# Kernel tuning notes

Hardware: AMD Instinct MI355X
Metric: run time of the kernel (lower is better)

Reference implementation:

```python
import jax, jax.numpy as jnp
import numpy as np

B, L, DIM, HEADS = 2, 2048, 1536, 12
HD = DIM // HEADS  # 128
C = HD // 2        # 64 rotary pairs
EPS = 1e-6


def setup_inputs() -> dict:
    key = jax.random.key(0)
    ks = jax.random.split(key, 8)
    x = jax.random.normal(ks[0], (B, L, DIM), jnp.float32)
    # ragged grids: sample0 fills L, sample1 has 2*24*32 = 1536 valid tokens
    grid_sizes = jnp.array([[2, 32, 32], [2, 24, 32]], dtype=jnp.int32)
    seq_lens = jnp.array([2048, 1536], dtype=jnp.int32)
    # rope freqs table [1024, C] (cos/sin of pos * inv_freq)
    pos = jnp.arange(1024, dtype=jnp.float32)[:, None]
    inv = 1.0 / (10000.0 ** (jnp.arange(C, dtype=jnp.float32) / C))
    ang = pos * inv
    freqs_cos, freqs_sin = jnp.cos(ang), jnp.sin(ang)
    init = lambda k: jax.random.normal(k, (DIM, DIM), jnp.float32) / np.sqrt(DIM)
    return dict(
        x=x, seq_lens=seq_lens, grid_sizes=grid_sizes,
        freqs_cos=freqs_cos, freqs_sin=freqs_sin,
        Wq=init(ks[1]), bq=jnp.zeros((DIM,), jnp.float32),
        Wk=init(ks[2]), bk=jnp.zeros((DIM,), jnp.float32),
        Wv=init(ks[3]), bv=jnp.zeros((DIM,), jnp.float32),
        Wo=init(ks[4]), bo=jnp.zeros((DIM,), jnp.float32),
        gq=jnp.ones((DIM,), jnp.float32), gk=jnp.ones((DIM,), jnp.float32),
    )


def _rope_one(xb, grid, cos, sin):
    # xb: [L, n, d]; grid: (f, h, w); cos/sin: [1024, C]
    f, h, w = grid[0], grid[1], grid[2]
    c = cos.shape[1]
    c2 = c // 3
    c1 = c - 2 * c2  # freqs split [c1, c2, c2] over axes (f, h, w)
    p = jnp.arange(xb.shape[0])
    hw = h * w
    valid = p < f * hw
    fi = jnp.where(valid, p // hw, 0)
    hi = jnp.where(valid, (p // w) % h, 0)
    wi = jnp.where(valid, p % w, 0)
    cos_p = jnp.concatenate([cos[fi, :c1], cos[hi, c1:c1 + c2], cos[wi, c1 + c2:]], axis=-1)
    sin_p = jnp.concatenate([sin[fi, :c1], sin[hi, c1:c1 + c2], sin[wi, c1 + c2:]], axis=-1)
    # positions beyond seq_len pass through unrotated (identity rotation)
    cos_p = jnp.where(valid[:, None], cos_p, 1.0)[:, None, :]  # [L,1,C]
    sin_p = jnp.where(valid[:, None], sin_p, 0.0)[:, None, :]
    xr, xi = xb[..., 0::2], xb[..., 1::2]
    out_r = xr * cos_p - xi * sin_p
    out_i = xr * sin_p + xi * cos_p
    return jnp.stack([out_r, out_i], axis=-1).reshape(xb.shape)


_rope_apply = jax.vmap(_rope_one, in_axes=(0, 0, None, None))


def _rms(t, g):
    t32 = t.astype(jnp.float32)
    return (t32 * jax.lax.rsqrt(jnp.mean(t32 * t32, axis=-1, keepdims=True) + EPS) * g).astype(t.dtype)


def reference(x, seq_lens, grid_sizes, freqs_cos, freqs_sin,
              Wq, bq, Wk, bk, Wv, bv, Wo, bo, gq, gk):
    b, s = x.shape[:2]
    n, d = HEADS, HD
    q = _rms(x @ Wq + bq, gq).reshape(b, s, n, d)
    k = _rms(x @ Wk + bk, gk).reshape(b, s, n, d)
    v = (x @ Wv + bv).reshape(b, s, n, d)
    q = _rope_apply(q, grid_sizes, freqs_cos, freqs_sin)
    k = _rope_apply(k, grid_sizes, freqs_cos, freqs_sin)
    scale = 1.0 / np.sqrt(d).astype(np.float32)
    scores = jnp.einsum('bqnd,bknd->bnqk', q, k) * scale
    kmask = jnp.arange(s)[None, :] < seq_lens[:, None]  # [b, s] key validity
    scores = jnp.where(kmask[:, None, None, :], scores, jnp.float32(-1e9))
    attn = jax.nn.softmax(scores, axis=-1)
    out = jnp.einsum('bnqk,bknd->bqnd', attn, v).reshape(b, s, n * d)
    return out @ Wo + bo
```

## Files before the change

### kernel.cpp

```cpp
#include <hip/hip_runtime.h>
#include <hip/hip_bf16.h>

#define DIM   1536
#define HEADS 12
#define HD    128
#define LSEQ  2048
#define NB    2
#define NTOK  (NB*LSEQ)

using f32x4 = __attribute__((ext_vector_type(4))) float;
using s16x8 = __attribute__((ext_vector_type(8))) short;
using u16x4 = __attribute__((ext_vector_type(4))) unsigned short;

__device__ __forceinline__ unsigned short f2bf(float f) {
  unsigned int u = __builtin_bit_cast(unsigned int, f);
  u += 0x7fffu + ((u >> 16) & 1u);
  return (unsigned short)(u >> 16);
}
__device__ __forceinline__ float bf2f(unsigned short u) {
  return __builtin_bit_cast(float, (unsigned int)u << 16);
}
__device__ __forceinline__ void gload_lds16(const void* g, void* l) {
  __builtin_amdgcn_global_load_lds(
      (__attribute__((address_space(1))) void*)const_cast<void*>(g),
      (__attribute__((address_space(3))) void*)l,
      16, 0, 0);
}

__global__ __launch_bounds__(256) void cvt_x(const float* __restrict__ x,
                                             unsigned short* __restrict__ xb, int n) {
  int i = (blockIdx.x * 256 + threadIdx.x) * 4;
  int stride = gridDim.x * 256 * 4;
  for (; i < n; i += stride) {
    f32x4 v = *(const f32x4*)(x + i);
    u16x4 o;
    o[0] = f2bf(v[0]); o[1] = f2bf(v[1]); o[2] = f2bf(v[2]); o[3] = f2bf(v[3]);
    *(u16x4*)(xb + i) = o;
  }
}

__global__ __launch_bounds__(256) void wtrans(const float* W0, const float* W1,
                                              const float* W2, const float* W3,
                                              unsigned short* __restrict__ Wt) {
  const float* W = blockIdx.z == 0 ? W0 : blockIdx.z == 1 ? W1 : blockIdx.z == 2 ? W2 : W3;
  unsigned short* out = Wt + (size_t)blockIdx.z * DIM * DIM;
  const int n0 = blockIdx.x * 64, k0 = blockIdx.y * 64;
  __shared__ unsigned short t[64][68];
  const int tid = threadIdx.x;
#pragma unroll
  for (int i = 0; i < 16; i++) {
    int idx = tid + i * 256;
    int r = idx >> 6, c = idx & 63;
    t[r][c] = f2bf(W[(size_t)(k0 + r) * DIM + n0 + c]);
  }
  __syncthreads();
#pragma unroll
  for (int i = 0; i < 16; i++) {
    int idx = tid + i * 256;
    int r = idx >> 6, c = idx & 63;
    out[(size_t)(n0 + r) * DIM + k0 + c] = t[c][r];
  }
}

__global__ __launch_bounds__(256) void gemm_bt(
    const unsigned short* __restrict__ A, const unsigned short* __restrict__ Bt,
    void* __restrict__ Cv,
    const float* __restrict__ b0, const float* __restrict__ b1, const float* __restrict__ b2,
    int M, int N, int K, int biasMode, int outBf16) {
  __shared__ __align__(16) unsigned short As[128 * 64];
  __shared__ __align__(16) unsigned short Bs[128 * 64];
  const int tid = threadIdx.x;
  const int lane = tid & 63, w = tid >> 6;
  const int wr = w >> 1, wc = w & 1;
  const int l15 = lane & 15, g4 = lane >> 4;
  const int nwg = gridDim.x * gridDim.y;
  const int bidf = blockIdx.y * gridDim.x + blockIdx.x;
  const int cpx = nwg >> 3;
  const int sw = (bidf & 7) * cpx + (bidf >> 3);
  const int m0 = (sw / gridDim.x) * 128, n0 = (sw % gridDim.x) * 128;

  f32x4 acc[4][4];
#pragma unroll
  for (int i = 0; i < 4; i++)
#pragma unroll
    for (int j = 0; j < 4; j++) acc[i][j] = (f32x4){0.f, 0.f, 0.f, 0.f};

  for (int kt = 0; kt < K; kt += 64) {
    __syncthreads();
#pragma unroll
    for (int i = 0; i < 4; i++) {
      int c = tid + i * 256;
      int row = c >> 3, g = c & 7;
      int gs = g ^ (row & 7);
      gload_lds16(A + (size_t)(m0 + row) * K + kt + gs * 8, As + c * 8);
    }
#pragma unroll
    for (int i = 0; i < 4; i++) {
      int c = tid + i * 256;
      int row = c >> 3, g = c & 7;
      int gs = g ^ (row & 7);
      gload_lds16(Bt + (size_t)(n0 + row) * K + kt + gs * 8, Bs + c * 8);
    }
    __syncthreads();
#pragma unroll
    for (int kk = 0; kk < 2; kk++) {
      s16x8 af[4], bfr[4];
#pragma unroll
      for (int m = 0; m < 4; m++) {
        int row = wr * 64 + m * 16 + l15;
        int off = row * 128 + ((kk * 64 + g4 * 16) ^ ((row & 7) << 4));
        af[m] = *(const s16x8*)((const char*)As + off);
      }
#pragma unroll
      for (int n = 0; n < 4; n++) {
        int row = wc * 64 + n * 16 + l15;
        int off = row * 128 + ((kk * 64 + g4 * 16) ^ ((row & 7) << 4));
        bfr[n] = *(const s16x8*)((const char*)Bs + off);
      }
#pragma unroll
      for (int m = 0; m < 4; m++)
#pragma unroll
        for (int n = 0; n < 4; n++)
          acc[m][n] = __builtin_amdgcn_mfma_f32_16x16x32_bf16(af[m], bfr[n], acc[m][n], 0, 0, 0);
    }
  }
#pragma unroll
  for (int m = 0; m < 4; m++)
#pragma unroll
    for (int n = 0; n < 4; n++)
#pragma unroll
      for (int r = 0; r < 4; r++) {
        int grow = m0 + wr * 64 + m * 16 + g4 * 4 + r;
        int gcol = n0 + wc * 64 + n * 16 + l15;
        float bias = (biasMode == 1)
                         ? b0[gcol]
                         : (gcol < 1536 ? b0[gcol]
                                        : (gcol < 3072 ? b1[gcol - 1536] : b2[gcol - 3072]));
        float val = acc[m][n][r] + bias;
        if (outBf16) ((unsigned short*)Cv)[(size_t)grow * N + gcol] = f2bf(val);
        else         ((float*)Cv)[(size_t)grow * N + gcol] = val;
      }
}

__global__ __launch_bounds__(256) void rmsrope(
    const unsigned short* __restrict__ qkvb,
    const float* __restrict__ gq, const float* __restrict__ gk,
    const int* __restrict__ grid_sizes,
    const float* __restrict__ fcos, const float* __restrict__ fsin,
    unsigned short* __restrict__ qb, unsigned short* __restrict__ kb) {
  const int t = blockIdx.x;
  const int b = t >> 11, l = t & 2047;
  const int tid = threadIdx.x;
  __shared__ float qrow[1536], krow[1536];
  __shared__ float red[8];
  const unsigned short* rq = qkvb + (size_t)t * 4608;
  const unsigned short* rk = rq + 1536;
  float sq = 0.f, sk = 0.f;
  if (tid < 192) {
    s16x8 vq = *(const s16x8*)(rq + tid * 8);
    s16x8 vk = *(const s16x8*)(rk + tid * 8);
#pragma unroll
    for (int j = 0; j < 8; j++) {
      float a = bf2f((unsigned short)vq[j]); qrow[tid * 8 + j] = a; sq += a * a;
      float c = bf2f((unsigned short)vk[j]); krow[tid * 8 + j] = c; sk += c * c;
    }
  }
  for (int o = 32; o; o >>= 1) { sq += __shfl_down(sq, o); sk += __shfl_down(sk, o); }
  if ((tid & 63) == 0) { red[tid >> 6] = sq; red[4 + (tid >> 6)] = sk; }
  __syncthreads();
  const float rsq = rsqrtf((red[0] + red[1] + red[2] + red[3]) * (1.f / 1536.f) + 1e-6f);
  const float rsk = rsqrtf((red[4] + red[5] + red[6] + red[7]) * (1.f / 1536.f) + 1e-6f);
  const float QS = 0.08838834764831845f;
  const int fg = grid_sizes[b * 3 + 0], hg = grid_sizes[b * 3 + 1], wg = grid_sizes[b * 3 + 2];
  const int hw = hg * wg;
  const bool valid = l < fg * hw;
  const int fi = valid ? l / hw : 0;
  const int hi = valid ? (l / wg) % hg : 0;
  const int wi = valid ? l % wg : 0;
  const size_t obase = (((size_t)b * HEADS) * LSEQ + l) * HD;
  for (int i = tid; i < HEADS * 64; i += 256) {
    int hd = i >> 6, j = i & 63;
    float c, s;
    if (valid) {
      int idx = j < 22 ? fi : (j < 43 ? hi : wi);
      c = fcos[idx * 64 + j]; s = fsin[idx * 64 + j];
    } else { c = 1.f; s = 0.f; }
    int col = hd * 128 + 2 * j;
    size_t o = obase + (size_t)hd * LSEQ * HD + 2 * j;
    float xr = qrow[col] * rsq * gq[col];
    float xi = qrow[col + 1] * rsq * gq[col + 1];
    float q0 = (xr * c - xi * s) * QS, q1 = (xr * s + xi * c) * QS;
    *(unsigned int*)(qb + o) = (unsigned int)f2bf(q0) | ((unsigned int)f2bf(q1) << 16);
    xr = krow[col] * rsk * gk[col];
    xi = krow[col + 1] * rsk * gk[col + 1];
    *(unsigned int*)(kb + o) =
        (unsigned int)f2bf(xr * c - xi * s) | ((unsigned int)f2bf(xr * s + xi * c) << 16);
  }
}

__global__ __launch_bounds__(256) void vtrans(const unsigned short* __restrict__ qkvb,
                                              unsigned short* __restrict__ vt) {
  const int lt = blockIdx.x, h = blockIdx.y, b = blockIdx.z;
  const int l0 = lt * 64;
  __shared__ unsigned short tile[64][130];
  const int tid = threadIdx.x;
#pragma unroll
  for (int i = 0; i < 4; i++) {
    int idx = tid + i * 256;
    int tk = idx >> 4, dc = (idx & 15) * 8;
    s16x8 v = *(const s16x8*)(qkvb + (size_t)(b * 2048 + l0 + tk) * 4608 + 3072 + h * 128 + dc);
#pragma unroll
    for (int j = 0; j < 8; j++) tile[tk][dc + j] = (unsigned short)v[j];
  }
  __syncthreads();
  const size_t ob = (((size_t)b * HEADS + h) * HD) * LSEQ + l0;
#pragma unroll
  for (int i = 0; i < 4; i++) {
    int idx = tid + i * 256;
    int d = idx >> 3, ck = (idx & 7) * 8;
    s16x8 o;
#pragma unroll
    for (int j = 0; j < 8; j++) o[j] = (short)tile[ck + j][d];
    *(s16x8*)(vt + ob + (size_t)d * LSEQ + ck) = o;
  }
}

__global__ __launch_bounds__(256) void flash(
    const unsigned short* __restrict__ qb, const unsigned short* __restrict__ kb,
    const unsigned short* __restrict__ vt, const int* __restrict__ seq_lens,
    unsigned short* __restrict__ ob) {
  const int qt = blockIdx.x, h = blockIdx.y, b = blockIdx.z;
  const int tid = threadIdx.x, lane = tid & 63, w = tid >> 6;
  const int l15 = lane & 15, g4 = lane >> 4;
  __shared__ __align__(16) unsigned short Ks[64 * 128];
  __shared__ __align__(16) unsigned short Vs[128 * 64];
  __shared__ __align__(16) unsigned short Pl[4][16 * 64];
  const size_t bh = (size_t)b * HEADS + h;
  const int q0 = qt * 64 + w * 16;
  s16x8 qf[4];
  {
    const unsigned short* qp = qb + (bh * LSEQ + q0 + l15) * HD;
#pragma unroll
    for (int c = 0; c < 4; c++) qf[c] = *(const s16x8*)(qp + c * 32 + g4 * 8);
  }
  union { unsigned short u[8]; s16x8 v; } ones_;
#pragma unroll
  for (int j = 0; j < 8; j++) ones_.u[j] = 0x3F80;

  f32x4 acc[9];
#pragma unroll
  for (int i = 0; i < 9; i++) acc[i] = (f32x4){0.f, 0.f, 0.f, 0.f};
  float mrow[4] = {-1e30f, -1e30f, -1e30f, -1e30f};
  const int ntile = seq_lens[b] >> 6;
  char* pw = (char*)&Pl[w][0];

#pragma unroll
  for (int i = 0; i < 4; i++) {
    int c = tid + i * 256, row = c >> 4, seg = c & 15, ss = seg ^ (row & 7);
    gload_lds16(kb + (bh * LSEQ + row) * HD + ss * 8, &Ks[0] + c * 8);
  }

  for (int kt = 0; kt < ntile; kt++) {
    const int k0 = kt * 64;
    __syncthreads();
#pragma unroll
    for (int i = 0; i < 4; i++) {
      int c = tid + i * 256, row = c >> 3, seg = c & 7, ss = seg ^ (row & 7);
      gload_lds16(vt + (bh * HD + row) * LSEQ + k0 + ss * 8, &Vs[0] + c * 8);
    }
    f32x4 sv[4];
    __builtin_amdgcn_s_setprio(1);
#pragma unroll
    for (int n = 0; n < 4; n++) {
      f32x4 a = (f32x4){0.f, 0.f, 0.f, 0.f};
      int key = n * 16 + l15;
#pragma unroll
      for (int c = 0; c < 4; c++) {
        int off = key * 256 + ((c * 64 + g4 * 16) ^ ((key & 7) << 4));
        s16x8 kf = *(const s16x8*)((const char*)Ks + off);
        a = __builtin_amdgcn_mfma_f32_16x16x32_bf16(qf[c], kf, a, 0, 0, 0);
      }
      sv[n] = a;
    }
    __builtin_amdgcn_s_setprio(0);
    float alpha_[4];
    bool anyGrow = false;
#pragma unroll
    for (int r = 0; r < 4; r++) {
      float v0 = sv[0][r], v1 = sv[1][r], v2 = sv[2][r], v3 = sv[3][r];
      float mx = fmaxf(fmaxf(v0, v1), fmaxf(v2, v3));
      unsigned long long vote = __ballot(mx > mrow[r] + 8.0f);
      bool grpGrow = ((vote >> (g4 * 16)) & 0xFFFFull) != 0;
      float mnew = mrow[r];
      float alpha = 1.f;
      if (grpGrow) {
#pragma unroll
        for (int o = 8; o; o >>= 1) mx = fmaxf(mx, __shfl_xor(mx, o));
        mnew = fmaxf(mrow[r], mx);
        alpha = __expf(mrow[r] - mnew);
      }
      float p0 = __expf(v0 - mnew), p1 = __expf(v1 - mnew);
      float p2 = __expf(v2 - mnew), p3 = __expf(v3 - mnew);
      mrow[r] = mnew; alpha_[r] = alpha; anyGrow |= grpGrow;
      int q = g4 * 4 + r;
      int swz = (q & 7) << 4;
      *(unsigned short*)(pw + q * 128 + ((2 * (0 * 16 + l15)) ^ swz)) = f2bf(p0);
      *(unsigned short*)(pw + q * 128 + ((2 * (1 * 16 + l15)) ^ swz)) = f2bf(p1);
      *(unsigned short*)(pw + q * 128 + ((2 * (2 * 16 + l15)) ^ swz)) = f2bf(p2);
      *(unsigned short*)(pw + q * 128 + ((2 * (3 * 16 + l15)) ^ swz)) = f2bf(p3);
    }
    if (__any((int)anyGrow)) {
#pragma unroll
      for (int dn = 0; dn < 9; dn++)
#pragma unroll
        for (int r = 0; r < 4; r++) acc[dn][r] *= alpha_[r];
    }
    __syncthreads();
    if (kt + 1 < ntile) {
#pragma unroll
      for (int i = 0; i < 4; i++) {
        int c = tid + i * 256, row = c >> 4, seg = c & 15, ss = seg ^ (row & 7);
        gload_lds16(kb + (bh * LSEQ + k0 + 64 + row) * HD + ss * 8, &Ks[0] + c * 8);
      }
    }
    s16x8 pa[2];
#pragma unroll
    for (int kk = 0; kk < 2; kk++) {
      int off = l15 * 128 + ((kk * 64 + g4 * 16) ^ ((l15 & 7) << 4));
      pa[kk] = *(const s16x8*)(pw + off);
    }
    __builtin_amdgcn_s_setprio(1);
#pragma unroll
    for (int dn = 0; dn < 8; dn++) {
      int d = dn * 16 + l15;
      int off0 = d * 128 + ((g4 * 16) ^ ((d & 7) << 4));
      int off1 = d * 128 + ((64 + g4 * 16) ^ ((d & 7) << 4));
      s16x8 vf0 = *(const s16x8*)((const char*)Vs + off0);
      s16x8 vf1 = *(const s16x8*)((const char*)Vs + off1);
      acc[dn] = __builtin_amdgcn_mfma_f32_16x16x32_bf16(pa[0], vf0, acc[dn], 0, 0, 0);
      acc[dn] = __builtin_amdgcn_mfma_f32_16x16x32_bf16(pa[1], vf1, acc[dn], 0, 0, 0);
    }
    acc[8] = __builtin_amdgcn_mfma_f32_16x16x32_bf16(pa[0], ones_.v, acc[8], 0, 0, 0);
    acc[8] = __builtin_amdgcn_mfma_f32_16x16x32_bf16(pa[1], ones_.v, acc[8], 0, 0, 0);
    __builtin_amdgcn_s_setprio(0);
  }
  float inv[4];
#pragma unroll
  for (int r = 0; r < 4; r++) inv[r] = 1.f / acc[8][r];
#pragma unroll
  for (int dn = 0; dn < 8; dn++)
#pragma unroll
    for (int r = 0; r < 4; r++) {
      int tok = b * LSEQ + qt * 64 + w * 16 + g4 * 4 + r;
      int col = h * HD + dn * 16 + l15;
      ob[(size_t)tok * DIM + col] = f2bf(acc[dn][r] * inv[r]);
    }
}

extern "C" void kernel_launch(void* const* d_in, const int* in_sizes, int n_in,
                              void* d_out, int out_size, void* d_ws, size_t ws_size,
                              hipStream_t stream) {
  const float* x    = (const float*)d_in[0];
  const int*   seq  = (const int*)d_in[1];
  const int*   grids= (const int*)d_in[2];
  const float* fcos = (const float*)d_in[3];
  const float* fsin = (const float*)d_in[4];
  const float* Wq   = (const float*)d_in[5];
  const float* bq   = (const float*)d_in[6];
  const float* Wk   = (const float*)d_in[7];
  const float* bk   = (const float*)d_in[8];
  const float* Wv   = (const float*)d_in[9];
  const float* bv   = (const float*)d_in[10];
  const float* Wo   = (const float*)d_in[11];
  const float* bo   = (const float*)d_in[12];
  const float* gq   = (const float*)d_in[13];
  const float* gk   = (const float*)d_in[14];

  char* ws = (char*)d_ws;
  unsigned short* xb   = (unsigned short*)(ws);
  unsigned short* Wt   = (unsigned short*)(ws + 12582912);
  unsigned short* qkvb = (unsigned short*)(ws + 31457280);
  unsigned short* qbb  = (unsigned short*)(ws + 69206016);
  unsigned short* kbb  = (unsigned short*)(ws + 81788928);
  unsigned short* vt   = (unsigned short*)d_out;
  unsigned short* obb  = xb;
  float* out = (float*)d_out;

  cvt_x<<<1024, 256, 0, stream>>>(x, xb, NTOK * DIM);
  wtrans<<<dim3(24, 24, 4), 256, 0, stream>>>(Wq, Wk, Wv, Wo, Wt);
  gemm_bt<<<dim3(36, 32), 256, 0, stream>>>(xb, Wt, qkvb, bq, bk, bv, NTOK, 3 * DIM, DIM, 0, 1);
  rmsrope<<<NTOK, 256, 0, stream>>>(qkvb, gq, gk, grids, fcos, fsin, qbb, kbb);
  vtrans<<<dim3(32, 12, 2), 256, 0, stream>>>(qkvb, vt);
  flash<<<dim3(32, 12, 2), 256, 0, stream>>>(qbb, kbb, vt, seq, obb);
  gemm_bt<<<dim3(12, 32), 256, 0, stream>>>(obb, Wt + (size_t)3 * DIM * DIM, out,
                                            bo, bo, bo, NTOK, DIM, DIM, 1, 0);
}
```

Measured before the change: 248.4 us.

## Double-buffer K/V tiles in flash attention with two-ahead prefetch

Splits the K and V shared-memory tiles into two buffers and prefetches tile kt+2 while computing on tile kt, replacing the per-iteration __syncthreads with explicit vmcnt waits and raw barriers. This is meant to hide global-to-LDS load latency behind the QK and PV MFMA work. It doubles LDS use for K/V, which may reduce occupancy, and issues redundant reloads near the end to keep the outstanding-load count consistent.

```diff
diff --git a/kernel.cpp b/kernel.cpp
--- a/kernel.cpp
+++ b/kernel.cpp
@@ -232,8 +232,8 @@
   const int qt = blockIdx.x, h = blockIdx.y, b = blockIdx.z;
   const int tid = threadIdx.x, lane = tid & 63, w = tid >> 6;
   const int l15 = lane & 15, g4 = lane >> 4;
-  __shared__ __align__(16) unsigned short Ks[64 * 128];
-  __shared__ __align__(16) unsigned short Vs[128 * 64];
+  __shared__ __align__(16) unsigned short Ks[2][64 * 128];
+  __shared__ __align__(16) unsigned short Vs[2][128 * 64];
   __shared__ __align__(16) unsigned short Pl[4][16 * 64];
   const size_t bh = (size_t)b * HEADS + h;
   const int q0 = qt * 64 + w * 16;
@@ -243,6 +243,9 @@
 #pragma unroll
     for (int c = 0; c < 4; c++) qf[c] = *(const s16x8*)(qp + c * 32 + g4 * 8);
   }
+  const int ntile = seq_lens[b] >> 6;
+  asm volatile("s_waitcnt vmcnt(0)" ::: "memory");
+
   union { unsigned short u[8]; s16x8 v; } ones_;
 #pragma unroll
   for (int j = 0; j < 8; j++) ones_.u[j] = 0x3F80;
@@ -251,23 +254,27 @@
 #pragma unroll
   for (int i = 0; i < 9; i++) acc[i] = (f32x4){0.f, 0.f, 0.f, 0.f};
   float mrow[4] = {-1e30f, -1e30f, -1e30f, -1e30f};
-  const int ntile = seq_lens[b] >> 6;
   char* pw = (char*)&Pl[w][0];
 
-#pragma unroll
-  for (int i = 0; i < 4; i++) {
-    int c = tid + i * 256, row = c >> 4, seg = c & 15, ss = seg ^ (row & 7);
-    gload_lds16(kb + (bh * LSEQ + row) * HD + ss * 8, &Ks[0] + c * 8);
-  }
+#define STAGE_K(T, BUF)                                                              \
+  _Pragma("unroll") for (int i = 0; i < 4; i++) {                                    \
+    int c = tid + i * 256, row = c >> 4, seg = c & 15, ss = seg ^ (row & 7);         \
+    gload_lds16(kb + (bh * LSEQ + (T) * 64 + row) * HD + ss * 8, &Ks[BUF][0] + c * 8); \
+  }
+#define STAGE_V(T, BUF)                                                              \
+  _Pragma("unroll") for (int i = 0; i < 4; i++) {                                    \
+    int c = tid + i * 256, row = c >> 3, seg = c & 7, ss = seg ^ (row & 7);          \
+    gload_lds16(vt + (bh * HD + row) * LSEQ + (T) * 64 + ss * 8, &Vs[BUF][0] + c * 8); \
+  }
+
+  STAGE_K(0, 0); STAGE_V(0, 0);
+  STAGE_K(1, 1); STAGE_V(1, 1);
 
   for (int kt = 0; kt < ntile; kt++) {
-    const int k0 = kt * 64;
-    __syncthreads();
-#pragma unroll
-    for (int i = 0; i < 4; i++) {
-      int c = tid + i * 256, row = c >> 3, seg = c & 7, ss = seg ^ (row & 7);
-      gload_lds16(vt + (bh * HD + row) * LSEQ + k0 + ss * 8, &Vs[0] + c * 8);
-    }
+    const int cur = kt & 1;
+    asm volatile("s_waitcnt vmcnt(16)" ::: "memory");
+    __builtin_amdgcn_s_barrier();
+    __builtin_amdgcn_sched_barrier(0);
     f32x4 sv[4];
     __builtin_amdgcn_s_setprio(1);
 #pragma unroll
@@ -277,7 +284,7 @@
 #pragma unroll
       for (int c = 0; c < 4; c++) {
         int off = key * 256 + ((c * 64 + g4 * 16) ^ ((key & 7) << 4));
-        s16x8 kf = *(const s16x8*)((const char*)Ks + off);
+        s16x8 kf = *(const s16x8*)((const char*)&Ks[cur][0] + off);
         a = __builtin_amdgcn_mfma_f32_16x16x32_bf16(qf[c], kf, a, 0, 0, 0);
       }
       sv[n] = a;
@@ -315,14 +322,6 @@
 #pragma unroll
         for (int r = 0; r < 4; r++) acc[dn][r] *= alpha_[r];
     }
-    __syncthreads();
-    if (kt + 1 < ntile) {
-#pragma unroll
-      for (int i = 0; i < 4; i++) {
-        int c = tid + i * 256, row = c >> 4, seg = c & 15, ss = seg ^ (row & 7);
-        gload_lds16(kb + (bh * LSEQ + k0 + 64 + row) * HD + ss * 8, &Ks[0] + c * 8);
-      }
-    }
     s16x8 pa[2];
 #pragma unroll
     for (int kk = 0; kk < 2; kk++) {
@@ -335,15 +334,25 @@
       int d = dn * 16 + l15;
       int off0 = d * 128 + ((g4 * 16) ^ ((d & 7) << 4));
       int off1 = d * 128 + ((64 + g4 * 16) ^ ((d & 7) << 4));
-      s16x8 vf0 = *(const s16x8*)((const char*)Vs + off0);
-      s16x8 vf1 = *(const s16x8*)((const char*)Vs + off1);
+      s16x8 vf0 = *(const s16x8*)((const char*)&Vs[cur][0] + off0);
+      s16x8 vf1 = *(const s16x8*)((const char*)&Vs[cur][0] + off1);
       acc[dn] = __builtin_amdgcn_mfma_f32_16x16x32_bf16(pa[0], vf0, acc[dn], 0, 0, 0);
       acc[dn] = __builtin_amdgcn_mfma_f32_16x16x32_bf16(pa[1], vf1, acc[dn], 0, 0, 0);
     }
     acc[8] = __builtin_amdgcn_mfma_f32_16x16x32_bf16(pa[0], ones_.v, acc[8], 0, 0, 0);
     acc[8] = __builtin_amdgcn_mfma_f32_16x16x32_bf16(pa[1], ones_.v, acc[8], 0, 0, 0);
     __builtin_amdgcn_s_setprio(0);
-  }
+    __builtin_amdgcn_s_barrier();
+    __builtin_amdgcn_sched_barrier(0);
+    if (kt + 2 < ntile) {
+      STAGE_K(kt + 2, cur); STAGE_V(kt + 2, cur);
+    } else if (kt < ntile - 1) {
+      STAGE_K(kt, cur); STAGE_V(kt, cur);
+    }
+  }
+  asm volatile("s_waitcnt vmcnt(0)" ::: "memory");
+#undef STAGE_K
+#undef STAGE_V
   float inv[4];
 #pragma unroll
   for (int r = 0; r < 4; r++) inv[r] = 1.f / acc[8][r];
```

Result: no change. 248.6 us (+0.1%).
